# Kernel tuning notes

Measured on AMD Instinct MI355X. Metric: run time of the kernel, lower is better.

Reference implementation:

```python
import jax, jax.numpy as jnp
import numpy as np

B, N, C_PTS = 16, 4096, 64
NPOINT, NSAMPLE = 1024, 32
MLP = [64, 64, 128]
IN_CH = 3 + C_PTS  # 67
EPS = 1e-5  # BatchNorm2d default eps


def setup_inputs() -> dict:
    key = jax.random.key(0)
    ks = jax.random.split(key, 2 + len(MLP))
    inp = {
        'xyz': jax.random.normal(ks[0], (B, N, 3), jnp.float32),
        'points': jax.random.normal(ks[1], (B, N, C_PTS), jnp.float32),
    }
    last = IN_CH
    for i, oc in enumerate(MLP):
        inp[f'W{i}'] = jax.random.normal(ks[2 + i], (oc, last), jnp.float32) * (1.0 / np.sqrt(last))
        inp[f'gamma{i}'] = jnp.ones((oc,), jnp.float32)
        inp[f'beta{i}'] = jnp.zeros((oc,), jnp.float32)
        last = oc
    return inp


def _farthest_point_sample(xyz, npoint):
    # xyz: (B, N, 3) -> (B, npoint) int32 indices. Sequential recurrence -> lax.scan.
    xyz = jax.lax.stop_gradient(xyz)
    b, n, _ = xyz.shape

    def step(carry, _):
        distance, farthest = carry
        centroid = jnp.take_along_axis(xyz, farthest[:, None, None], axis=1)  # (B,1,3)
        dist = jnp.sum((xyz - centroid) ** 2, axis=-1)  # (B,N)
        distance = jnp.minimum(distance, dist)
        farthest_next = jnp.argmax(distance, axis=-1).astype(jnp.int32)
        return (distance, farthest_next), farthest

    init = (jnp.full((b, n), jnp.inf, dtype=xyz.dtype), jnp.zeros((b,), jnp.int32))
    _, centroids = jax.lax.scan(step, init, None, length=npoint)  # (npoint, B)
    return centroids.T  # (B, npoint)


def _square_distance(src, dst):
    # src (B,S,3), dst (B,N,3) -> (B,S,N)
    src2 = jnp.sum(src * src, axis=-1, keepdims=True)            # (B,S,1)
    dst2 = jnp.sum(dst * dst, axis=-1, keepdims=True)            # (B,N,1)
    return src2 - 2.0 * jnp.einsum('bsc,bnc->bsn', src, dst) + jnp.swapaxes(dst2, 1, 2)


def _knn(k, xyz, new_xyz):
    dist = _square_distance(jax.lax.stop_gradient(new_xyz), jax.lax.stop_gradient(xyz))
    _, idx = jax.lax.top_k(-dist, k)  # smallest distances
    return idx  # (B,S,k) int32


def _gather(points, idx):
    # points (B,N,C); idx (B,S) or (B,S,K)
    return jax.vmap(lambda p, i: p[i])(points, idx)


def reference(xyz, points, W0, gamma0, beta0, W1, gamma1, beta1, W2, gamma2, beta2):
    fps_idx = _farthest_point_sample(xyz, NPOINT)           # (B,S)
    new_xyz = _gather(xyz, fps_idx)                          # (B,S,3)
    idx = _knn(NSAMPLE, xyz, new_xyz)                        # (B,S,K)
    grouped_xyz = _gather(xyz, idx)                          # (B,S,K,3)
    grouped_xyz_norm = grouped_xyz - new_xyz[:, :, None, :]
    grouped_points = _gather(points, idx)                    # (B,S,K,C)
    x = jnp.concatenate([grouped_xyz_norm, grouped_points], axis=-1)  # (B,S,K,Cin)

    for W, g, b in ((W0, gamma0, beta0), (W1, gamma1, beta1), (W2, gamma2, beta2)):
        x = jnp.einsum('bskc,oc->bsko', x, W)                # 1x1 conv
        mu = jnp.mean(x, axis=(0, 1, 2))                     # training-mode BN stats
        var = jnp.var(x, axis=(0, 1, 2))
        x = jax.nn.relu((x - mu) * jax.lax.rsqrt(var + EPS) * g + b)

    x = jnp.max(x, axis=2)                                   # max over nsample -> (B,S,Cout)
    return (new_xyz, x)
```

## Files before the change

### kernel.cpp

```cpp
#include <hip/hip_runtime.h>
#include <stdint.h>

#define B_    16
#define N_    4096
#define CPTS  64
#define S_    1024
#define K_    32

typedef __bf16 bf16x8 __attribute__((ext_vector_type(8)));
typedef float  f32x4  __attribute__((ext_vector_type(4)));
typedef unsigned short ushort8 __attribute__((ext_vector_type(8)));

__device__ __forceinline__ float fmul_(float a, float b){ return __fmul_rn(a,b); }
__device__ __forceinline__ float fadd_(float a, float b){ return __fadd_rn(a,b); }
__device__ __forceinline__ float fsub_(float a, float b){ return __fsub_rn(a,b); }

__device__ __forceinline__ unsigned short f2bf(float f){
  unsigned u = __float_as_uint(f);
  unsigned r = (u + 0x7FFFu + ((u >> 16) & 1u)) >> 16;
  return (unsigned short)r;
}

__device__ __forceinline__ f32x4 mfma_16x16x32(bf16x8 a, bf16x8 b, f32x4 c){
  return __builtin_amdgcn_mfma_f32_16x16x32_bf16(a, b, c, 0, 0, 0);
}

__device__ __forceinline__ unsigned long long umin64(unsigned long long a, unsigned long long b){
  return b < a ? b : a;
}
__device__ __forceinline__ unsigned long long umax64(unsigned long long a, unsigned long long b){
  return a < b ? b : a;
}

template<int CTRL>
__device__ __forceinline__ unsigned dppmove(unsigned v){
  return (unsigned)__builtin_amdgcn_update_dpp((int)v, (int)v, CTRL, 0xF, 0xF, false);
}
__device__ __forceinline__ unsigned wave_umax_dpp(unsigned v){
  unsigned t;
  t = dppmove<0x111>(v); v = v > t ? v : t;
  t = dppmove<0x112>(v); v = v > t ? v : t;
  t = dppmove<0x114>(v); v = v > t ? v : t;
  t = dppmove<0x118>(v); v = v > t ? v : t;
  t = dppmove<0x142>(v); v = v > t ? v : t;
  t = dppmove<0x143>(v); v = v > t ? v : t;
  return (unsigned)__builtin_amdgcn_readlane((int)v, 63);
}

__global__ __launch_bounds__(256) void fps_kernel(const float* __restrict__ xyz,
                                                  float* __restrict__ out_newxyz)
{
  const int b   = blockIdx.x;
  const int tid = threadIdx.x;
  const int wave = tid >> 6;
  __shared__ float4 lp[N_];
  __shared__ unsigned long long wc[2][4];
  __shared__ int fhist[S_ + 1];

  const float* xb = xyz + (size_t)b * (N_*3);
  float px[16], py[16], pz[16], dmin[16];
#pragma unroll
  for (int i = 0; i < 16; ++i) {
    int n = i*256 + tid;
    float x = xb[n*3+0], y = xb[n*3+1], z = xb[n*3+2];
    lp[n] = make_float4(x,y,z,0.0f);
    px[i]=x; py[i]=y; pz[i]=z;
    dmin[i] = INFINITY;
  }
  if (tid == 0) fhist[0] = 0;
  __syncthreads();

  int far = 0;
  for (int step = 0; step < S_; ++step) {
    float4 cp = lp[far];
    float cx = cp.x, cy = cp.y, cz = cp.z;
    float bv = -1.0f; unsigned bidx = 0;
#pragma unroll
    for (int i = 0; i < 16; ++i) {
      float dx = fsub_(px[i],cx), dy = fsub_(py[i],cy), dz = fsub_(pz[i],cz);
      float d  = fadd_(fadd_(fmul_(dx,dx),fmul_(dy,dy)),fmul_(dz,dz));
      float dm = fminf(dmin[i], d);
      dmin[i] = dm;
      bool gt = dm > bv;
      bv   = gt ? dm : bv;
      bidx = gt ? (unsigned)(i*256 + tid) : bidx;
    }
    unsigned bvb  = __float_as_uint(bv);
    unsigned wmax = wave_umax_dpp(bvb);
    unsigned cand = (bvb == wmax) ? ~bidx : 0u;
    unsigned winv = wave_umax_dpp(cand);
    unsigned long long kv = ((unsigned long long)wmax << 32) | winv;

    int par = step & 1;
    if ((tid & 63) == 0) wc[par][wave] = kv;
    __syncthreads();
    unsigned long long b0 = umax64(wc[par][0], wc[par][1]);
    unsigned long long b1 = umax64(wc[par][2], wc[par][3]);
    far = (int)(~(unsigned)umax64(b0, b1));
    if (tid == 0) fhist[step + 1] = far;
  }
  __syncthreads();

  float* ob = out_newxyz + (size_t)b*S_*3;
#pragma unroll
  for (int j = 0; j < 4; ++j) {
    int s = j*256 + tid;
    float4 p = lp[fhist[s]];
    ob[s*3+0] = p.x; ob[s*3+1] = p.y; ob[s*3+2] = p.z;
  }
}

#define KNN_REB(G) { \
  if (isw) { \
    if      (jj==0u) sk[(G)*8+0]=0xFFFFFFFFu; else if (jj==1u) sk[(G)*8+1]=0xFFFFFFFFu; \
    else if (jj==2u) sk[(G)*8+2]=0xFFFFFFFFu; else if (jj==3u) sk[(G)*8+3]=0xFFFFFFFFu; \
    else if (jj==4u) sk[(G)*8+4]=0xFFFFFFFFu; else if (jj==5u) sk[(G)*8+5]=0xFFFFFFFFu; \
    else if (jj==6u) sk[(G)*8+6]=0xFFFFFFFFu; else              sk[(G)*8+7]=0xFFFFFFFFu; } \
  { unsigned bk = sk[(G)*8+0]; unsigned bi = (unsigned)(((G)*8+0)*64 + lane); \
    _Pragma("unroll") \
    for (int j2 = 1; j2 < 8; ++j2) { \
      unsigned k2 = sk[(G)*8+j2]; unsigned i2 = (unsigned)(((G)*8+j2)*64 + lane); \
      bool lt = k2 < bk; bk = lt ? k2 : bk; bi = lt ? i2 : bi; } \
    gk[(G)] = bk; gi[(G)] = bi; } }

__global__ __launch_bounds__(256) void knn_kernel(const float* __restrict__ xyz,
                                                  const float* __restrict__ newxyz,
                                                  int* __restrict__ knn)
{
  __shared__ float4 lp[N_];
  const int b     = blockIdx.x >> 6;
  const int chunk = blockIdx.x & 63;
  const float* xb = xyz + (size_t)b * (N_*3);
  for (int e = threadIdx.x; e < N_; e += 256) {
    float x = xb[e*3+0], y = xb[e*3+1], z = xb[e*3+2];
    float d2 = fadd_(fadd_(fmul_(x,x),fmul_(y,y)),fmul_(z,z));
    lp[e] = make_float4(x,y,z,d2);
  }
  __syncthreads();

  const int wave = threadIdx.x >> 6, lane = threadIdx.x & 63;
  for (int qi = 0; qi < 4; ++qi) {
    const int s  = chunk*16 + wave*4 + qi;
    const int fq = b*S_ + s;
    float qx = newxyz[fq*3+0], qy = newxyz[fq*3+1], qz = newxyz[fq*3+2];
    float s2 = fadd_(fadd_(fmul_(qx,qx),fmul_(qy,qy)),fmul_(qz,qz));

    unsigned sk[64];
#pragma unroll
    for (int j = 0; j < 64; ++j) {
      float4 p = lp[j*64 + lane];
      float dot = fadd_(fadd_(fmul_(qx,p.x),fmul_(qy,p.y)),fmul_(qz,p.z));
      float d   = fadd_(fsub_(s2, fmul_(2.0f,dot)), p.w);
      unsigned u = __float_as_uint(d);
      sk[j] = u ^ ((unsigned)((int)u >> 31) | 0x80000000u);
    }
    unsigned gk[8], gi[8];
#pragma unroll
    for (int g = 0; g < 8; ++g) {
      unsigned bk = sk[g*8+0], bi = (unsigned)((g*8+0)*64 + lane);
#pragma unroll
      for (int j = 1; j < 8; ++j) {
        unsigned k2 = sk[g*8+j]; unsigned i2 = (unsigned)((g*8+j)*64 + lane);
        bool lt = k2 < bk; bk = lt ? k2 : bk; bi = lt ? i2 : bi;
      }
      gk[g]=bk; gi[g]=bi;
    }
    int* ko = knn + (size_t)fq * K_;
    for (int it = 0; it < K_; ++it) {
      unsigned long long c0 = ((unsigned long long)gk[0] << 32) | gi[0];
      unsigned long long c1 = ((unsigned long long)gk[1] << 32) | gi[1];
      unsigned long long c2 = ((unsigned long long)gk[2] << 32) | gi[2];
      unsigned long long c3 = ((unsigned long long)gk[3] << 32) | gi[3];
      unsigned long long c4 = ((unsigned long long)gk[4] << 32) | gi[4];
      unsigned long long c5 = ((unsigned long long)gk[5] << 32) | gi[5];
      unsigned long long c6 = ((unsigned long long)gk[6] << 32) | gi[6];
      unsigned long long c7 = ((unsigned long long)gk[7] << 32) | gi[7];
      c0 = umin64(c0,c1); c2 = umin64(c2,c3); c4 = umin64(c4,c5); c6 = umin64(c6,c7);
      c0 = umin64(c0,c2); c4 = umin64(c4,c6);
      unsigned long long cand = umin64(c0,c4);
#pragma unroll
      for (int m = 1; m <= 32; m <<= 1) {
        unsigned long long o = __shfl_xor(cand, m, 64);
        cand = (o < cand) ? o : cand;
      }
      unsigned widx = (unsigned)cand;
      if (lane == 0) ko[it] = (int)widx;
      unsigned wl = widx & 63u, wj = widx >> 6;
      unsigned g = wj >> 3, jj = wj & 7u;
      bool isw = (lane == (int)wl);
      switch (g) {
        case 0: KNN_REB(0); break;
        case 1: KNN_REB(1); break;
        case 2: KNN_REB(2); break;
        case 3: KNN_REB(3); break;
        case 4: KNN_REB(4); break;
        case 5: KNN_REB(5); break;
        case 6: KNN_REB(6); break;
        default: KNN_REB(7); break;
      }
    }
  }
}

template<int KS, int NT>
__device__ __forceinline__ void layer_mfma(const unsigned short* A, const unsigned short* W,
                                           int wstride, f32x4 (&acc)[2][NT], int wave, int lane)
{
  const int quad = lane >> 4, row0 = lane & 15;
  bf16x8 a[2][KS];
#pragma unroll
  for (int m2 = 0; m2 < 2; ++m2)
#pragma unroll
    for (int ks = 0; ks < KS; ++ks)
      a[m2][ks] = *(const bf16x8*)&A[((wave*2+m2)*16 + row0)*104 + ks*32 + quad*8];
#pragma unroll
  for (int m2 = 0; m2 < 2; ++m2)
#pragma unroll
    for (int n = 0; n < NT; ++n)
      acc[m2][n] = (f32x4){0.f,0.f,0.f,0.f};
#pragma unroll
  for (int n = 0; n < NT; ++n) {
#pragma unroll
    for (int ks = 0; ks < KS; ++ks) {
      bf16x8 bfrag = *(const bf16x8*)&W[(n*16 + row0)*wstride + ks*32 + quad*8];
      acc[0][n] = mfma_16x16x32(a[0][ks], bfrag, acc[0][n]);
      acc[1][n] = mfma_16x16x32(a[1][ks], bfrag, acc[1][n]);
    }
  }
}

template<int NT>
__device__ __forceinline__ void stats_ep(const f32x4 (&acc)[2][NT], float* sum, float* sq, int lane)
{
  const int part = blockIdx.x & 63;
  const int col0 = lane & 15;
#pragma unroll
  for (int n = 0; n < NT; ++n) {
    float s = 0.f, q = 0.f;
#pragma unroll
    for (int m2 = 0; m2 < 2; ++m2)
#pragma unroll
      for (int t = 0; t < 4; ++t) { float z = acc[m2][n][t]; s += z; q += z*z; }
    s += __shfl_xor(s, 16, 64); q += __shfl_xor(q, 16, 64);
    s += __shfl_xor(s, 32, 64); q += __shfl_xor(q, 32, 64);
    if (lane < 16) {
      atomicAdd(&sum[part*128 + n*16 + col0], s);
      atomicAdd(&sq [part*128 + n*16 + col0], q);
    }
  }
}

template<int NT>
__device__ __forceinline__ void bn_store(const f32x4 (&acc)[2][NT], unsigned short* A,
                                         const float* lmu, const float* lrsg, const float* lbeta,
                                         int off, int wave, int quad, int col0)
{
#pragma unroll
  for (int n = 0; n < NT; ++n) {
    int c = n*16 + col0;
    float mu = lmu[off+c], rg = lrsg[off+c], bt = lbeta[off+c];
#pragma unroll
    for (int m2 = 0; m2 < 2; ++m2)
#pragma unroll
      for (int t = 0; t < 4; ++t) {
        int row = (wave*2+m2)*16 + quad*4 + t;
        float v = fmaxf((acc[m2][n][t] - mu)*rg + bt, 0.0f);
        A[row*104 + c] = f2bf(v);
      }
  }
}

template<int STAGE>
__global__ __launch_bounds__(256) void mlp_kernel(
    const float* __restrict__ xyz, const float* __restrict__ pts,
    const float* __restrict__ W0, const float* __restrict__ g0, const float* __restrict__ be0,
    const float* __restrict__ W1, const float* __restrict__ g1, const float* __restrict__ be1,
    const float* __restrict__ W2, const float* __restrict__ g2, const float* __restrict__ be2,
    const float* __restrict__ newxyz, const int* __restrict__ knn,
    float* __restrict__ stats, float* __restrict__ out1)
{
  __shared__ unsigned short sA[128*104];
  __shared__ unsigned short wb[128*72];
  __shared__ float lmu[256], lrsg[256], lbeta[256];

  const int tid  = threadIdx.x;
  const int wave = tid >> 6, lane = tid & 63;
  const int quad = lane >> 4, col0 = lane & 15;

  {
    const int nl = STAGE - 1;
    const int   couts[3] = {64,64,128};
    const int   offs[3]  = {0,64,128};
    const float* gs[3]   = {g0,g1,g2};
    const float* bs[3]   = {be0,be1,be2};
    for (int l = 0; l < nl; ++l) {
      if (tid < couts[l]) {
        const float* su = stats + (size_t)(2*l)*8192;
        const float* sq = stats + (size_t)(2*l+1)*8192;
        float sm = 0.f, q = 0.f;
        for (int p = 0; p < 64; ++p) { sm += su[p*128+tid]; q += sq[p*128+tid]; }
        float mu  = sm * (1.0f/524288.0f);
        float var = q  * (1.0f/524288.0f) - mu*mu;
        float rs  = rsqrtf(var + 1e-5f);
        lmu [offs[l]+tid] = mu;
        lrsg[offs[l]+tid] = rs * gs[l][tid];
        lbeta[offs[l]+tid] = bs[l][tid];
      }
    }
  }

  {
    const int r = tid >> 1, half = tid & 1;
    const int ql = r >> 5, kk = r & 31;
    const int fq = blockIdx.x*4 + ql;
    const int b  = fq >> 10;
    const int p  = knn[(size_t)fq*K_ + kk];
    const float4* p4 = (const float4*)(pts + ((size_t)(b<<12) + p) * CPTS);
    ushort8* arow = (ushort8*)&sA[r*104];
    if (half == 0) {
#pragma unroll
      for (int ch = 0; ch < 4; ++ch) {
        float4 a = p4[ch*2], bq = p4[ch*2+1];
        ushort8 v = { f2bf(a.x),f2bf(a.y),f2bf(a.z),f2bf(a.w),
                      f2bf(bq.x),f2bf(bq.y),f2bf(bq.z),f2bf(bq.w) };
        arow[ch] = v;
      }
    } else {
#pragma unroll
      for (int ch = 4; ch < 8; ++ch) {
        float4 a = p4[ch*2], bq = p4[ch*2+1];
        ushort8 v = { f2bf(a.x),f2bf(a.y),f2bf(a.z),f2bf(a.w),
                      f2bf(bq.x),f2bf(bq.y),f2bf(bq.z),f2bf(bq.w) };
        arow[ch] = v;
      }
      const float* xr = xyz + ((size_t)(b<<12) + p)*3;
      float qx = newxyz[fq*3+0], qy = newxyz[fq*3+1], qz = newxyz[fq*3+2];
      ushort8 vx = { f2bf(fsub_(xr[0],qx)), f2bf(fsub_(xr[1],qy)), f2bf(fsub_(xr[2],qz)),
                     0,0,0,0,0 };
      arow[8] = vx;
      ushort8 z = {0,0,0,0,0,0,0,0};
      arow[9] = z; arow[10] = z; arow[11] = z;
    }
  }

  {
    const int n = tid >> 2, q = tid & 3;
    const float* wr = W0 + n*67;
#pragma unroll
    for (int ch = 0; ch < 3; ++ch) {
      int c0 = q*24 + ch*8;
      ushort8 v;
#pragma unroll
      for (int j = 0; j < 8; ++j) {
        int cc = c0 + j;
        float f = (cc < 64) ? wr[3+cc] : ((cc < 67) ? wr[cc-64] : 0.0f);
        v[j] = f2bf(f);
      }
      *(ushort8*)&wb[n*104 + c0] = v;
    }
  }
  __syncthreads();

  f32x4 acc0[2][4];
  layer_mfma<3,4>(sA, wb, 104, acc0, wave, lane);
  __syncthreads();
  if constexpr (STAGE == 1) { stats_ep<4>(acc0, stats + 0*8192, stats + 1*8192, lane); return; }

  bn_store<4>(acc0, sA, lmu, lrsg, lbeta, 0, wave, quad, col0);
  {
    const int n = tid >> 2, k0 = (tid & 3) * 16;
    const float4* w4 = (const float4*)(W1 + n*64 + k0);
#pragma unroll
    for (int i = 0; i < 2; ++i) {
      float4 a = w4[i*2], bq = w4[i*2+1];
      ushort8 v = { f2bf(a.x),f2bf(a.y),f2bf(a.z),f2bf(a.w),
                    f2bf(bq.x),f2bf(bq.y),f2bf(bq.z),f2bf(bq.w) };
      ((ushort8*)&wb[n*72 + k0])[i] = v;
    }
  }
  __syncthreads();

  f32x4 acc1[2][4];
  layer_mfma<2,4>(sA, wb, 72, acc1, wave, lane);
  __syncthreads();
  if constexpr (STAGE == 2) { stats_ep<4>(acc1, stats + 2*8192, stats + 3*8192, lane); return; }

  bn_store<4>(acc1, sA, lmu, lrsg, lbeta, 64, wave, quad, col0);
  {
    const int n = tid >> 1, k0 = (tid & 1) * 32;
    const float4* w4 = (const float4*)(W2 + n*64 + k0);
#pragma unroll
    for (int i = 0; i < 4; ++i) {
      float4 a = w4[i*2], bq = w4[i*2+1];
      ushort8 v = { f2bf(a.x),f2bf(a.y),f2bf(a.z),f2bf(a.w),
                    f2bf(bq.x),f2bf(bq.y),f2bf(bq.z),f2bf(bq.w) };
      ((ushort8*)&wb[n*72 + k0])[i] = v;
    }
  }
  __syncthreads();

  f32x4 acc2[2][8];
  layer_mfma<2,8>(sA, wb, 72, acc2, wave, lane);
  if constexpr (STAGE == 3) { stats_ep<8>(acc2, stats + 4*8192, stats + 5*8192, lane); return; }

  {
    const int fq = blockIdx.x*4 + wave;
#pragma unroll
    for (int n = 0; n < 8; ++n) {
      int c = n*16 + col0;
      float mu = lmu[128+c], rg = lrsg[128+c], bt = lbeta[128+c];
      float mx = -INFINITY;
#pragma unroll
      for (int m2 = 0; m2 < 2; ++m2)
#pragma unroll
        for (int t = 0; t < 4; ++t) {
          float v = fmaxf((acc2[m2][n][t] - mu)*rg + bt, 0.0f);
          mx = fmaxf(mx, v);
        }
      mx = fmaxf(mx, __shfl_xor(mx, 16, 64));
      mx = fmaxf(mx, __shfl_xor(mx, 32, 64));
      if (lane < 16) out1[(size_t)fq*128 + c] = mx;
    }
  }
}

extern "C" void kernel_launch(void* const* d_in, const int* in_sizes, int n_in,
                              void* d_out, int out_size, void* d_ws, size_t ws_size,
                              hipStream_t stream)
{
  (void)in_sizes; (void)n_in; (void)out_size; (void)ws_size;
  const float* xyz  = (const float*)d_in[0];
  const float* pts  = (const float*)d_in[1];
  const float* W0   = (const float*)d_in[2];
  const float* g0   = (const float*)d_in[3];
  const float* be0  = (const float*)d_in[4];
  const float* W1   = (const float*)d_in[5];
  const float* g1   = (const float*)d_in[6];
  const float* be1  = (const float*)d_in[7];
  const float* W2   = (const float*)d_in[8];
  const float* g2   = (const float*)d_in[9];
  const float* be2  = (const float*)d_in[10];

  float* out  = (float*)d_out;
  float* out1 = out + (size_t)B_*S_*3;
  int*   knn   = (int*)d_ws;
  float* stats = (float*)((char*)d_ws + (size_t)B_*S_*K_*4);

  hipMemsetAsync(stats, 0, (size_t)6*8192*sizeof(float), stream);
  fps_kernel<<<16, 256, 0, stream>>>(xyz, out);
  knn_kernel<<<1024, 256, 0, stream>>>(xyz, out, knn);
  mlp_kernel<1><<<4096, 256, 0, stream>>>(xyz, pts, W0,g0,be0, W1,g1,be1, W2,g2,be2, out, knn, stats, out1);
  mlp_kernel<2><<<4096, 256, 0, stream>>>(xyz, pts, W0,g0,be0, W1,g1,be1, W2,g2,be2, out, knn, stats, out1);
  mlp_kernel<3><<<4096, 256, 0, stream>>>(xyz, pts, W0,g0,be0, W1,g1,be1, W2,g2,be2, out, knn, stats, out1);
  mlp_kernel<4><<<4096, 256, 0, stream>>>(xyz, pts, W0,g0,be0, W1,g1,be1, W2,g2,be2, out, knn, stats, out1);
}
```

Before: 1.351 ms.

## Materialize bf16 layer outputs to workspace instead of recomputing earlier MLP layers

```diff
diff --git a/kernel.cpp b/kernel.cpp
--- a/kernel.cpp
+++ b/kernel.cpp
@@ -19,6 +19,9 @@
   unsigned u = __float_as_uint(f);
   unsigned r = (u + 0x7FFFu + ((u >> 16) & 1u)) >> 16;
   return (unsigned short)r;
+}
+__device__ __forceinline__ float bf2f(unsigned short u){
+  return __uint_as_float((unsigned)u << 16);
 }
 
 __device__ __forceinline__ f32x4 mfma_16x16x32(bf16x8 a, bf16x8 b, f32x4 c){
@@ -270,6 +273,279 @@
   }
 }
 
+template<int NT, int STRIDE>
+__device__ __forceinline__ void pre_store(const f32x4 (&acc)[2][NT], unsigned short* A,
+                                          int wave, int quad, int col0)
+{
+#pragma unroll
+  for (int n = 0; n < NT; ++n) {
+    int c = n*16 + col0;
+#pragma unroll
+    for (int m2 = 0; m2 < 2; ++m2)
+#pragma unroll
+      for (int t = 0; t < 4; ++t) {
+        int row = (wave*2+m2)*16 + quad*4 + t;
+        A[row*STRIDE + c] = f2bf(acc[m2][n][t]);
+      }
+  }
+}
+
+__device__ __forceinline__ void load_bn_layer(const float* stats, const float* g, const float* be,
+                                              int L, int cout, float* lmu, float* lrsg, float* lbeta,
+                                              int tid)
+{
+  if (tid < cout) {
+    const float* su = stats + (size_t)(2*L)*8192;
+    const float* sq = stats + (size_t)(2*L+1)*8192;
+    float sm = 0.f, q = 0.f;
+    for (int p = 0; p < 64; ++p) { sm += su[p*128+tid]; q += sq[p*128+tid]; }
+    float mu  = sm * (1.0f/524288.0f);
+    float var = q  * (1.0f/524288.0f) - mu*mu;
+    float rs  = rsqrtf(var + 1e-5f);
+    lmu[tid]  = mu;
+    lrsg[tid] = rs * g[tid];
+    lbeta[tid]= be[tid];
+  }
+}
+
+__device__ __forceinline__ void gather_tile(const float* xyz, const float* pts,
+                                            const float* newxyz, const int* knn,
+                                            unsigned short* sA, int tid)
+{
+  const int r = tid >> 1, half = tid & 1;
+  const int ql = r >> 5, kk = r & 31;
+  const int fq = blockIdx.x*4 + ql;
+  const int b  = fq >> 10;
+  const int p  = knn[(size_t)fq*K_ + kk];
+  const float4* p4 = (const float4*)(pts + ((size_t)(b<<12) + p) * CPTS);
+  ushort8* arow = (ushort8*)&sA[r*104];
+  if (half == 0) {
+#pragma unroll
+    for (int ch = 0; ch < 4; ++ch) {
+      float4 a = p4[ch*2], bq = p4[ch*2+1];
+      ushort8 v = { f2bf(a.x),f2bf(a.y),f2bf(a.z),f2bf(a.w),
+                    f2bf(bq.x),f2bf(bq.y),f2bf(bq.z),f2bf(bq.w) };
+      arow[ch] = v;
+    }
+  } else {
+#pragma unroll
+    for (int ch = 4; ch < 8; ++ch) {
+      float4 a = p4[ch*2], bq = p4[ch*2+1];
+      ushort8 v = { f2bf(a.x),f2bf(a.y),f2bf(a.z),f2bf(a.w),
+                    f2bf(bq.x),f2bf(bq.y),f2bf(bq.z),f2bf(bq.w) };
+      arow[ch] = v;
+    }
+    const float* xr = xyz + ((size_t)(b<<12) + p)*3;
+    float qx = newxyz[fq*3+0], qy = newxyz[fq*3+1], qz = newxyz[fq*3+2];
+    ushort8 vx = { f2bf(fsub_(xr[0],qx)), f2bf(fsub_(xr[1],qy)), f2bf(fsub_(xr[2],qz)),
+                   0,0,0,0,0 };
+    arow[8] = vx;
+    ushort8 z = {0,0,0,0,0,0,0,0};
+    arow[9] = z; arow[10] = z; arow[11] = z;
+  }
+}
+
+__device__ __forceinline__ void load_w0(const float* W0, unsigned short* wb, int tid)
+{
+  const int n = tid >> 2, q = tid & 3;
+  const float* wr = W0 + n*67;
+#pragma unroll
+  for (int ch = 0; ch < 3; ++ch) {
+    int c0 = q*24 + ch*8;
+    ushort8 v;
+#pragma unroll
+    for (int j = 0; j < 8; ++j) {
+      int cc = c0 + j;
+      float f = (cc < 64) ? wr[3+cc] : ((cc < 67) ? wr[cc-64] : 0.0f);
+      v[j] = f2bf(f);
+    }
+    *(ushort8*)&wb[n*104 + c0] = v;
+  }
+}
+
+__device__ __forceinline__ void load_w1(const float* W1, unsigned short* wb, int tid)
+{
+  const int n = tid >> 2, k0 = (tid & 3) * 16;
+  const float4* w4 = (const float4*)(W1 + n*64 + k0);
+#pragma unroll
+  for (int i = 0; i < 2; ++i) {
+    float4 a = w4[i*2], bq = w4[i*2+1];
+    ushort8 v = { f2bf(a.x),f2bf(a.y),f2bf(a.z),f2bf(a.w),
+                  f2bf(bq.x),f2bf(bq.y),f2bf(bq.z),f2bf(bq.w) };
+    ((ushort8*)&wb[n*72 + k0])[i] = v;
+  }
+}
+
+__device__ __forceinline__ void load_w2(const float* W2, unsigned short* wb, int tid)
+{
+  const int n = tid >> 1, k0 = (tid & 1) * 32;
+  const float4* w4 = (const float4*)(W2 + n*64 + k0);
+#pragma unroll
+  for (int i = 0; i < 4; ++i) {
+    float4 a = w4[i*2], bq = w4[i*2+1];
+    ushort8 v = { f2bf(a.x),f2bf(a.y),f2bf(a.z),f2bf(a.w),
+                  f2bf(bq.x),f2bf(bq.y),f2bf(bq.z),f2bf(bq.w) };
+    ((ushort8*)&wb[n*72 + k0])[i] = v;
+  }
+}
+
+__global__ __launch_bounds__(256) void mlpA_kernel(
+    const float* __restrict__ xyz, const float* __restrict__ pts,
+    const float* __restrict__ W0,
+    const float* __restrict__ newxyz, const int* __restrict__ knn,
+    float* __restrict__ stats, unsigned short* __restrict__ z0)
+{
+  __shared__ unsigned short sA[128*104];
+  __shared__ unsigned short wb[128*104];
+  const int tid  = threadIdx.x;
+  const int wave = tid >> 6, lane = tid & 63;
+  const int quad = lane >> 4, col0 = lane & 15;
+
+  gather_tile(xyz, pts, newxyz, knn, sA, tid);
+  load_w0(W0, wb, tid);
+  __syncthreads();
+
+  f32x4 acc0[2][4];
+  layer_mfma<3,4>(sA, wb, 104, acc0, wave, lane);
+  stats_ep<4>(acc0, stats + 0*8192, stats + 1*8192, lane);
+  __syncthreads();
+  pre_store<4,104>(acc0, sA, wave, quad, col0);
+  __syncthreads();
+
+  const int r = tid >> 1, hf = tid & 1;
+  const ushort8* src = (const ushort8*)&sA[r*104 + hf*32];
+  ushort8* dst = (ushort8*)(z0 + (size_t)blockIdx.x*8192 + r*64 + hf*32);
+#pragma unroll
+  for (int i = 0; i < 4; ++i) dst[i] = src[i];
+}
+
+template<int LPREV, int COUT_PREV>
+__device__ __forceinline__ void stage_in(const unsigned short* zin,
+                                         const float* stats, const float* g, const float* be,
+                                         unsigned short* sA, float* lmu, float* lrsg, float* lbeta,
+                                         int tid)
+{
+  const int r = tid >> 1, hf = tid & 1;
+  const unsigned short* zp = zin + (size_t)blockIdx.x*8192 + r*64 + hf*32;
+  ushort8 in[4];
+#pragma unroll
+  for (int i = 0; i < 4; ++i) in[i] = ((const ushort8*)zp)[i];
+  load_bn_layer(stats, g, be, LPREV, COUT_PREV, lmu, lrsg, lbeta, tid);
+  __syncthreads();
+#pragma unroll
+  for (int i = 0; i < 4; ++i) {
+    ushort8 v;
+#pragma unroll
+    for (int j = 0; j < 8; ++j) {
+      int c = hf*32 + i*8 + j;
+      float f = bf2f(in[i][j]);
+      float x = fmaxf((f - lmu[c])*lrsg[c] + lbeta[c], 0.0f);
+      v[j] = f2bf(x);
+    }
+    ((ushort8*)&sA[r*104 + hf*32])[i] = v;
+  }
+}
+
+__global__ __launch_bounds__(256) void mlpB_kernel(
+    const float* __restrict__ g0, const float* __restrict__ be0,
+    const float* __restrict__ W1,
+    float* __restrict__ stats,
+    const unsigned short* __restrict__ z0, unsigned short* __restrict__ z1)
+{
+  __shared__ unsigned short sA[128*104];
+  __shared__ unsigned short wb[128*72];
+  __shared__ float lmu[64], lrsg[64], lbeta[64];
+  const int tid  = threadIdx.x;
+  const int wave = tid >> 6, lane = tid & 63;
+  const int quad = lane >> 4, col0 = lane & 15;
+
+  load_w1(W1, wb, tid);
+  stage_in<0,64>(z0, stats, g0, be0, sA, lmu, lrsg, lbeta, tid);
+  __syncthreads();
+
+  f32x4 acc1[2][4];
+  layer_mfma<2,4>(sA, wb, 72, acc1, wave, lane);
+  stats_ep<4>(acc1, stats + 2*8192, stats + 3*8192, lane);
+  __syncthreads();
+  pre_store<4,104>(acc1, sA, wave, quad, col0);
+  __syncthreads();
+
+  const int r = tid >> 1, hf = tid & 1;
+  const ushort8* src = (const ushort8*)&sA[r*104 + hf*32];
+  ushort8* dst = (ushort8*)(z1 + (size_t)blockIdx.x*8192 + r*64 + hf*32);
+#pragma unroll
+  for (int i = 0; i < 4; ++i) dst[i] = src[i];
+}
+
+__global__ __launch_bounds__(256) void mlpC_kernel(
+    const float* __restrict__ g1, const float* __restrict__ be1,
+    const float* __restrict__ W2,
+    float* __restrict__ stats,
+    const unsigned short* __restrict__ z1, unsigned short* __restrict__ z2)
+{
+  __shared__ unsigned short BUF[22528];
+  __shared__ float lmu[64], lrsg[64], lbeta[64];
+  unsigned short* sA = BUF;
+  unsigned short* wb = BUF + 13312;
+  const int tid  = threadIdx.x;
+  const int wave = tid >> 6, lane = tid & 63;
+  const int quad = lane >> 4, col0 = lane & 15;
+
+  load_w2(W2, wb, tid);
+  stage_in<1,64>(z1, stats, g1, be1, sA, lmu, lrsg, lbeta, tid);
+  __syncthreads();
+
+  f32x4 acc2[2][8];
+  layer_mfma<2,8>(sA, wb, 72, acc2, wave, lane);
+  stats_ep<8>(acc2, stats + 4*8192, stats + 5*8192, lane);
+  __syncthreads();
+  pre_store<8,136>(acc2, BUF, wave, quad, col0);
+  __syncthreads();
+
+  const int r = tid >> 1, hf = tid & 1;
+  const ushort8* src = (const ushort8*)&BUF[r*136 + hf*64];
+  ushort8* dst = (ushort8*)(z2 + (size_t)blockIdx.x*16384 + r*128 + hf*64);
+#pragma unroll
+  for (int i = 0; i < 8; ++i) dst[i] = src[i];
+}
+
+typedef unsigned short ushort4v __attribute__((ext_vector_type(4)));
+
+__global__ __launch_bounds__(256) void mlpD_kernel(
+    const float* __restrict__ g2, const float* __restrict__ be2,
+    const float* __restrict__ stats,
+    const unsigned short* __restrict__ z2, float* __restrict__ out1)
+{
+  __shared__ float lmu[128], lrsg[128], lbeta[128];
+  const int tid = threadIdx.x;
+  load_bn_layer(stats, g2, be2, 2, 128, lmu, lrsg, lbeta, tid);
+  __syncthreads();
+
+  const int wq = tid >> 5, l32 = tid & 31;
+  const int fq = blockIdx.x*8 + wq;
+  const int tile = fq >> 2, ql = fq & 3;
+  const int c0 = l32 * 4;
+  const unsigned short* zp = z2 + ((size_t)tile*128 + ql*32)*128 + c0;
+
+  float mu[4], rg[4], bt[4], mx[4];
+#pragma unroll
+  for (int j = 0; j < 4; ++j) {
+    mu[j] = lmu[c0+j]; rg[j] = lrsg[c0+j]; bt[j] = lbeta[c0+j];
+    mx[j] = -INFINITY;
+  }
+  for (int r = 0; r < 32; ++r) {
+    ushort4v v = *(const ushort4v*)(zp + (size_t)r*128);
+#pragma unroll
+    for (int j = 0; j < 4; ++j) {
+      float f = bf2f(v[j]);
+      float x = fmaxf((f - mu[j])*rg[j] + bt[j], 0.0f);
+      mx[j] = fmaxf(mx[j], x);
+    }
+  }
+  float4 o = make_float4(mx[0], mx[1], mx[2], mx[3]);
+  *(float4*)(out1 + (size_t)fq*128 + c0) = o;
+}
+
 template<int STAGE>
 __global__ __launch_bounds__(256) void mlp_kernel(
     const float* __restrict__ xyz, const float* __restrict__ pts,
@@ -280,7 +556,7 @@
     float* __restrict__ stats, float* __restrict__ out1)
 {
   __shared__ unsigned short sA[128*104];
-  __shared__ unsigned short wb[128*72];
+  __shared__ unsigned short wb[128*104];
   __shared__ float lmu[256], lrsg[256], lbeta[256];
 
   const int tid  = threadIdx.x;
@@ -309,56 +585,8 @@
     }
   }
 
-  {
-    const int r = tid >> 1, half = tid & 1;
-    const int ql = r >> 5, kk = r & 31;
-    const int fq = blockIdx.x*4 + ql;
-    const int b  = fq >> 10;
-    const int p  = knn[(size_t)fq*K_ + kk];
-    const float4* p4 = (const float4*)(pts + ((size_t)(b<<12) + p) * CPTS);
-    ushort8* arow = (ushort8*)&sA[r*104];
-    if (half == 0) {
-#pragma unroll
-      for (int ch = 0; ch < 4; ++ch) {
-        float4 a = p4[ch*2], bq = p4[ch*2+1];
-        ushort8 v = { f2bf(a.x),f2bf(a.y),f2bf(a.z),f2bf(a.w),
-                      f2bf(bq.x),f2bf(bq.y),f2bf(bq.z),f2bf(bq.w) };
-        arow[ch] = v;
-      }
-    } else {
-#pragma unroll
-      for (int ch = 4; ch < 8; ++ch) {
-        float4 a = p4[ch*2], bq = p4[ch*2+1];
-        ushort8 v = { f2bf(a.x),f2bf(a.y),f2bf(a.z),f2bf(a.w),
-                      f2bf(bq.x),f2bf(bq.y),f2bf(bq.z),f2bf(bq.w) };
-        arow[ch] = v;
-      }
-      const float* xr = xyz + ((size_t)(b<<12) + p)*3;
-      float qx = newxyz[fq*3+0], qy = newxyz[fq*3+1], qz = newxyz[fq*3+2];
-      ushort8 vx = { f2bf(fsub_(xr[0],qx)), f2bf(fsub_(xr[1],qy)), f2bf(fsub_(xr[2],qz)),
-                     0,0,0,0,0 };
-      arow[8] = vx;
-      ushort8 z = {0,0,0,0,0,0,0,0};
-      arow[9] = z; arow[10] = z; arow[11] = z;
-    }
-  }
-
-  {
-    const int n = tid >> 2, q = tid & 3;
-    const float* wr = W0 + n*67;
-#pragma unroll
-    for (int ch = 0; ch < 3; ++ch) {
-      int c0 = q*24 + ch*8;
-      ushort8 v;
-#pragma unroll
-      for (int j = 0; j < 8; ++j) {
-        int cc = c0 + j;
-        float f = (cc < 64) ? wr[3+cc] : ((cc < 67) ? wr[cc-64] : 0.0f);
-        v[j] = f2bf(f);
-      }
-      *(ushort8*)&wb[n*104 + c0] = v;
-    }
-  }
+  gather_tile(xyz, pts, newxyz, knn, sA, tid);
+  load_w0(W0, wb, tid);
   __syncthreads();
 
   f32x4 acc0[2][4];
@@ -367,17 +595,7 @@
   if constexpr (STAGE == 1) { stats_ep<4>(acc0, stats + 0*8192, stats + 1*8192, lane); return; }
 
   bn_store<4>(acc0, sA, lmu, lrsg, lbeta, 0, wave, quad, col0);
-  {
-    const int n = tid >> 2, k0 = (tid & 3) * 16;
-    const float4* w4 = (const float4*)(W1 + n*64 + k0);
-#pragma unroll
-    for (int i = 0; i < 2; ++i) {
-      float4 a = w4[i*2], bq = w4[i*2+1];
-      ushort8 v = { f2bf(a.x),f2bf(a.y),f2bf(a.z),f2bf(a.w),
-                    f2bf(bq.x),f2bf(bq.y),f2bf(bq.z),f2bf(bq.w) };
-      ((ushort8*)&wb[n*72 + k0])[i] = v;
-    }
-  }
+  load_w1(W1, wb, tid);
   __syncthreads();
 
   f32x4 acc1[2][4];
@@ -386,17 +604,7 @@
   if constexpr (STAGE == 2) { stats_ep<4>(acc1, stats + 2*8192, stats + 3*8192, lane); return; }
 
   bn_store<4>(acc1, sA, lmu, lrsg, lbeta, 64, wave, quad, col0);
-  {
-    const int n = tid >> 1, k0 = (tid & 1) * 32;
-    const float4* w4 = (const float4*)(W2 + n*64 + k0);
-#pragma unroll
-    for (int i = 0; i < 4; ++i) {
-      float4 a = w4[i*2], bq = w4[i*2+1];
-      ushort8 v = { f2bf(a.x),f2bf(a.y),f2bf(a.z),f2bf(a.w),
-                    f2bf(bq.x),f2bf(bq.y),f2bf(bq.z),f2bf(bq.w) };
-      ((ushort8*)&wb[n*72 + k0])[i] = v;
-    }
-  }
+  load_w2(W2, wb, tid);
   __syncthreads();
 
   f32x4 acc2[2][8];
@@ -428,7 +636,7 @@
                               void* d_out, int out_size, void* d_ws, size_t ws_size,
                               hipStream_t stream)
 {
-  (void)in_sizes; (void)n_in; (void)out_size; (void)ws_size;
+  (void)in_sizes; (void)n_in; (void)out_size;
   const float* xyz  = (const float*)d_in[0];
   const float* pts  = (const float*)d_in[1];
   const float* W0   = (const float*)d_in[2];
@@ -443,14 +651,33 @@
 
   float* out  = (float*)d_out;
   float* out1 = out + (size_t)B_*S_*3;
-  int*   knn   = (int*)d_ws;
-  float* stats = (float*)((char*)d_ws + (size_t)B_*S_*K_*4);
+
+  const size_t knn_off   = 0;
+  const size_t stats_off = 2097152;
+  const size_t z0_off    = 2293760;
+  const size_t z1_off    = z0_off + 67108864;
+  const size_t z2_off    = z1_off + 67108864;
+  const size_t need      = z2_off + 134217728;
+
+  int*   knn   = (int*)((char*)d_ws + knn_off);
+  float* stats = (float*)((char*)d_ws + stats_off);
 
   hipMemsetAsync(stats, 0, (size_t)6*8192*sizeof(float), stream);
   fps_kernel<<<16, 256, 0, stream>>>(xyz, out);
   knn_kernel<<<1024, 256, 0, stream>>>(xyz, out, knn);
-  mlp_kernel<1><<<4096, 256, 0, stream>>>(xyz, pts, W0,g0,be0, W1,g1,be1, W2,g2,be2, out, knn, stats, out1);
-  mlp_kernel<2><<<4096, 256, 0, stream>>>(xyz, pts, W0,g0,be0, W1,g1,be1, W2,g2,be2, out, knn, stats, out1);
-  mlp_kernel<3><<<4096, 256, 0, stream>>>(xyz, pts, W0,g0,be0, W1,g1,be1, W2,g2,be2, out, knn, stats, out1);
-  mlp_kernel<4><<<4096, 256, 0, stream>>>(xyz, pts, W0,g0,be0, W1,g1,be1, W2,g2,be2, out, knn, stats, out1);
-}
+
+  if (ws_size >= need) {
+    unsigned short* z0 = (unsigned short*)((char*)d_ws + z0_off);
+    unsigned short* z1 = (unsigned short*)((char*)d_ws + z1_off);
+    unsigned short* z2 = (unsigned short*)((char*)d_ws + z2_off);
+    mlpA_kernel<<<4096, 256, 0, stream>>>(xyz, pts, W0, out, knn, stats, z0);
+    mlpB_kernel<<<4096, 256, 0, stream>>>(g0, be0, W1, stats, z0, z1);
+    mlpC_kernel<<<4096, 256, 0, stream>>>(g1, be1, W2, stats, z1, z2);
+    mlpD_kernel<<<2048, 256, 0, stream>>>(g2, be2, stats, z2, out1);
+  } else {
+    mlp_kernel<1><<<4096, 256, 0, stream>>>(xyz, pts, W0,g0,be0, W1,g1,be1, W2,g2,be2, out, knn, stats, out1);
+    mlp_kernel<2><<<4096, 256, 0, stream>>>(xyz, pts, W0,g0,be0, W1,g1,be1, W2,g2,be2, out, knn, stats, out1);
+    mlp_kernel<3><<<4096, 256, 0, stream>>>(xyz, pts, W0,g0,be0, W1,g1,be1, W2,g2,be2, out, knn, stats, out1);
+    mlp_kernel<4><<<4096, 256, 0, stream>>>(xyz, pts, W0,g0,be0, W1,g1,be1, W2,g2,be2, out, knn, stats, out1);
+  }
+}
```

Result: slower. 1.391 ms (+2.9%).
